# Kernel optimization log

Measured on AMD Instinct MI355X. Metric: run time of the kernel, lower is better.

The kernel has to match this reference:

```python
import jax, jax.numpy as jnp
import numpy as np

EPS = 1e-7  # K.epsilon()
ROUTINGS = 3
NUM_CAPSULE = 32
DIM_CAPSULE = 64


def squash(x, axis=-1):
    # NOTE: faithful to the source: x / sqrt(sum(x^2) + eps) (no squash factor)
    s = jnp.sum(jnp.square(x), axis=axis, keepdims=True)
    return x / jnp.sqrt(s + EPS)


def setup_inputs() -> dict:
    key = jax.random.key(0)
    k1, k2 = jax.random.split(key)
    B, I, C = 32, 1024, 256
    u_vecs = jax.random.normal(k1, (B, I, C), dtype=jnp.float32)
    # glorot-ish scale for the capsule kernel (1x1 conv == matmul C -> N*D)
    W = jax.random.normal(k2, (C, NUM_CAPSULE * DIM_CAPSULE), dtype=jnp.float32) * 0.03
    return {"u_vecs": u_vecs, "W": W}


def reference(u_vecs, W):
    B, I, C = u_vecs.shape
    N, D = NUM_CAPSULE, DIM_CAPSULE
    # conv1d with kernel size 1 == matmul; reshape + permute to (B, N, I, D)
    u_hat = jnp.einsum('bic,ce->bie', u_vecs, W)  # (B, I, N*D)
    u_hat = u_hat.reshape(B, I, N, D).transpose(0, 2, 1, 3)  # (B, N, I, D)

    b = jnp.zeros((B, N, I), dtype=u_hat.dtype)
    outputs = None
    for i in range(ROUTINGS):
        c = jax.nn.softmax(b, axis=1)  # softmax over num_capsule axis
        outputs = squash(jnp.einsum('bni,bnid->bnd', c, u_hat))  # (B, N, D)
        if i < ROUTINGS - 1:
            b = jnp.einsum('bnd,bnid->bni', outputs, u_hat)
    return outputs
```

## Files before the change

### kernel.cpp

```cpp
#include <hip/hip_runtime.h>
#include <math.h>


constexpr int Bn = 32, In = 1024, Cn = 256, Nn = 32, Dn = 64, ND = 2048;

typedef __attribute__((ext_vector_type(8))) short bf16x8;
typedef __attribute__((ext_vector_type(4))) float f32x4;

__device__ __forceinline__ unsigned int packbf2(float a, float b) {
  unsigned int xa = __float_as_uint(a), xb = __float_as_uint(b);
  xa = (xa + 0x7fffu + ((xa >> 16) & 1u)) >> 16;
  xb = (xb + 0x7fffu + ((xb >> 16) & 1u)) >> 16;
  return xa | (xb << 16);
}
__device__ __forceinline__ unsigned short packbf1(float a) {
  unsigned int x = __float_as_uint(a);
  return (unsigned short)((x + 0x7fffu + ((x >> 16) & 1u)) >> 16);
}
__device__ __forceinline__ float bfu(unsigned short us) {
  return __uint_as_float((unsigned int)us << 16);
}

__global__ __launch_bounds__(256) void k_pre(
    const float* __restrict__ u, const float* __restrict__ W,
    float* __restrict__ psu, unsigned short* __restrict__ Wbf,
    unsigned short* __restrict__ WbfT, unsigned short* __restrict__ ub16) {
  const int z = blockIdx.x, tid = threadIdx.x;
  if (z < 1024) {
    int b = z >> 5, ch = z & 31;
    const float* up = u + ((size_t)(b * In + ch * 32)) * Cn + tid;
    unsigned short* ubp = ub16 + ((size_t)(b * In + ch * 32)) * Cn + tid;
    float s = 0.f;
#pragma unroll 8
    for (int j = 0; j < 32; ++j) {
      float v = up[(size_t)j * Cn];
      s += v;
      ubp[(size_t)j * Cn] = packbf1(v);
    }
    psu[(size_t)z * Cn + tid] = s;
  } else if (z < 1152) {
    __shared__ float tile[64][65];
    int t = z - 1024;
    int x0 = (t & 31) * 64, y0 = (t >> 5) * 64;
    int lx = tid & 63, ly = tid >> 6;
#pragma unroll
    for (int k = 0; k < 16; ++k) {
      int y = ly + k * 4;
      tile[y][lx] = W[(size_t)(y0 + y) * ND + x0 + lx];
    }
    __syncthreads();
#pragma unroll
    for (int k = 0; k < 8; ++k) {
      int idx = tid + k * 256;
      int row = idx >> 5, cu = idx & 31;
      unsigned int v = packbf2(tile[2 * cu][row], tile[2 * cu + 1][row]);
      *(unsigned int*)&WbfT[(size_t)(x0 + row) * Cn + y0 + 2 * cu] = v;
    }
  } else {
    int zb = z - 1152;
    const float* src = W + (size_t)zb * 4096;
    unsigned short* dst = Wbf + (size_t)zb * 4096;
#pragma unroll
    for (int k = 0; k < 4; ++k) {
      int off = k * 1024 + tid * 4;
      const float4 v = *(const float4*)&src[off];
      *(uint2*)&dst[off] = make_uint2(packbf2(v.x, v.y), packbf2(v.z, v.w));
    }
  }
}

__global__ __launch_bounds__(256) void k_sst(
    const void* __restrict__ src, int srcBf16, long bS, long nS, long cS,
    float scale, const unsigned short* __restrict__ Wbf,
    const unsigned short* __restrict__ WbfT, unsigned short* __restrict__ tb,
    float* __restrict__ outp, int writeT) {
  int bn = blockIdx.x, b = bn >> 5, n = bn & 31;
  int tid = threadIdx.x;
  __shared__ float vs[Cn];
  __shared__ float ol[Dn];
  __shared__ float scr[2176];
  {
    const int g = tid >> 5, co = tid & 31;
    float acc[8];
#pragma unroll
    for (int e = 0; e < 8; ++e) acc[e] = 0.f;
    if (srcBf16) {
      const unsigned short* p =
          (const unsigned short*)src + b * bS + n * nS + co * 8;
#pragma unroll
      for (int k = 0; k < 4; ++k) {
        union { bf16x8 v; unsigned short us[8]; } w;
        w.v = *(const bf16x8*)&p[(size_t)(g * 4 + k) * cS];
#pragma unroll
        for (int e = 0; e < 8; ++e) acc[e] += bfu(w.us[e]);
      }
    } else {
      const float* p = (const float*)src + b * bS + n * nS + co * 8;
#pragma unroll
      for (int k = 0; k < 4; ++k) {
        const float4 v0 = *(const float4*)&p[(size_t)(g * 4 + k) * cS];
        const float4 v1 = *(const float4*)&p[(size_t)(g * 4 + k) * cS + 4];
        acc[0] += v0.x; acc[1] += v0.y; acc[2] += v0.z; acc[3] += v0.w;
        acc[4] += v1.x; acc[5] += v1.y; acc[6] += v1.z; acc[7] += v1.w;
      }
    }
    *(float4*)&scr[g * 272 + co * 8] =
        make_float4(acc[0], acc[1], acc[2], acc[3]);
    *(float4*)&scr[g * 272 + co * 8 + 4] =
        make_float4(acc[4], acc[5], acc[6], acc[7]);
  }
  __syncthreads();
  {
    float s = 0.f;
#pragma unroll
    for (int k = 0; k < 8; ++k) s += scr[k * 272 + tid];
    vs[tid] = s * scale;
  }
  __syncthreads();
  {
    const int cg = tid >> 3, do8 = tid & 7;
    const unsigned short* wp =
        Wbf + (size_t)(cg * 8) * ND + (size_t)n * Dn + do8 * 8;
    float acc[8];
#pragma unroll
    for (int e = 0; e < 8; ++e) acc[e] = 0.f;
#pragma unroll
    for (int j = 0; j < 8; ++j) {
      union { bf16x8 v; unsigned short us[8]; } w;
      w.v = *(const bf16x8*)&wp[(size_t)j * ND];
      const float vc = vs[cg * 8 + j];
#pragma unroll
      for (int e = 0; e < 8; ++e) acc[e] += vc * bfu(w.us[e]);
    }
    *(float4*)&scr[cg * 68 + do8 * 8] =
        make_float4(acc[0], acc[1], acc[2], acc[3]);
    *(float4*)&scr[cg * 68 + do8 * 8 + 4] =
        make_float4(acc[4], acc[5], acc[6], acc[7]);
  }
  __syncthreads();
  if (tid < 64) {
    float a = 0.f;
#pragma unroll
    for (int k = 0; k < 32; ++k) a += scr[k * 68 + tid];
    float sq = a * a;
#pragma unroll
    for (int off = 32; off > 0; off >>= 1) sq += __shfl_xor(sq, off, 64);
    float o = a / sqrtf(sq + 1e-7f);
    ol[tid] = o;
    if (outp) outp[(size_t)bn * Dn + tid] = o;
  }
  __syncthreads();
  if (writeT) {
    {
      const int dg = tid >> 5, co = tid & 31;
      const unsigned short* wt =
          WbfT + (size_t)(n * Dn + dg * 8) * Cn + co * 8;
      float acc[8];
#pragma unroll
      for (int e = 0; e < 8; ++e) acc[e] = 0.f;
#pragma unroll
      for (int e = 0; e < 8; ++e) {
        union { bf16x8 v; unsigned short us[8]; } w;
        w.v = *(const bf16x8*)&wt[(size_t)e * Cn];
        const float od = ol[dg * 8 + e];
#pragma unroll
        for (int cc = 0; cc < 8; ++cc) acc[cc] += od * bfu(w.us[cc]);
      }
      *(float4*)&scr[dg * 272 + co * 8] =
          make_float4(acc[0], acc[1], acc[2], acc[3]);
      *(float4*)&scr[dg * 272 + co * 8 + 4] =
          make_float4(acc[4], acc[5], acc[6], acc[7]);
    }
    __syncthreads();
    {
      float s = 0.f;
#pragma unroll
      for (int k = 0; k < 8; ++k) s += scr[k * 272 + tid];
      tb[(size_t)bn * Cn + tid] = packbf1(s);
    }
  }
}

__global__ __launch_bounds__(256, 4) void k_route(
    const unsigned short* __restrict__ tbb,
    const unsigned short* __restrict__ ub16,
    unsigned short* __restrict__ pvb) {
  const int b = blockIdx.x, itile = blockIdx.y, i0 = itile * 32;
  const int tid = threadIdx.x;
  const int lane = tid & 63, w = tid >> 6;
  const int mrow = lane & 15, quad = lane >> 4;

  __shared__ unsigned short t_l[32][264];
  __shared__ unsigned short u_t[256][40];
  __shared__ unsigned short cm_l[32][40];
  __shared__ float bb_l[32][36];
  __shared__ float smr[2][8][32];

  {
    const unsigned short* tp = tbb + (size_t)b * Nn * Cn;
#pragma unroll
    for (int k = 0; k < 8; ++k) {
      int idx = tid + k * 256;
      int row = idx >> 6, q = idx & 63;
      *(uint2*)&t_l[row][q * 4] = *(const uint2*)&tp[(size_t)row * Cn + q * 4];
    }
    const int ti = tid & 31, qb = tid >> 5;
    const unsigned short* up = ub16 + ((size_t)(b * In + i0 + ti)) * Cn;
#pragma unroll
    for (int m = 0; m < 4; ++m) {
      int c8 = qb + m * 8;
      union { bf16x8 v; unsigned short us[8]; } uv;
      uv.v = *(const bf16x8*)&up[c8 * 8];
#pragma unroll
      for (int e = 0; e < 8; ++e) u_t[c8 * 8 + e][ti] = uv.us[e];
    }
  }
  __syncthreads();

  {
    const int i0t = (w & 1) * 16, n0t = (w >> 1) * 16;
    const unsigned short* ubp =
        ub16 + ((size_t)(b * In + i0 + i0t + mrow)) * Cn + quad * 8;
    f32x4 acc = {0.f, 0.f, 0.f, 0.f};
#pragma unroll
    for (int k0 = 0; k0 < 8; ++k0) {
      const bf16x8 af = *(const bf16x8*)(ubp + k0 * 32);
      const bf16x8 bf = *(const bf16x8*)&t_l[n0t + mrow][k0 * 32 + quad * 8];
      acc = __builtin_amdgcn_mfma_f32_16x16x32_bf16(af, bf, acc, 0, 0, 0);
    }
#pragma unroll
    for (int r = 0; r < 4; ++r)
      bb_l[n0t + mrow][i0t + quad * 4 + r] = acc[r];
  }
  __syncthreads();

  {
    const int i = tid & 31, g = tid >> 5;
    float m4 = bb_l[g * 4 + 0][i];
    m4 = fmaxf(m4, bb_l[g * 4 + 1][i]);
    m4 = fmaxf(m4, bb_l[g * 4 + 2][i]);
    m4 = fmaxf(m4, bb_l[g * 4 + 3][i]);
    smr[0][g][i] = m4;
    __syncthreads();
    float m = smr[0][0][i];
#pragma unroll
    for (int k = 1; k < 8; ++k) m = fmaxf(m, smr[0][k][i]);
    float s4 = 0.f;
#pragma unroll
    for (int r = 0; r < 4; ++r) {
      float e = __expf(bb_l[g * 4 + r][i] - m);
      bb_l[g * 4 + r][i] = e;
      s4 += e;
    }
    smr[1][g][i] = s4;
    __syncthreads();
    float ss = 0.f;
#pragma unroll
    for (int k = 0; k < 8; ++k) ss += smr[1][k][i];
    float inv = 1.f / ss;
#pragma unroll
    for (int r = 0; r < 4; ++r) bb_l[g * 4 + r][i] *= inv;
  }
  __syncthreads();

  {
    int n = tid >> 3, q = tid & 7;
    const float4 cv = *(const float4*)&bb_l[n][q * 4];
    *(uint2*)&cm_l[n][q * 4] = make_uint2(packbf2(cv.x, cv.y), packbf2(cv.z, cv.w));
  }
  __syncthreads();

  unsigned short* pvs = &t_l[0][0];
  {
    const int mt = w & 1;
    const bf16x8 af = *(const bf16x8*)&cm_l[mt * 16 + mrow][quad * 8];
#pragma unroll
    for (int j = 0; j < 8; ++j) {
      const int ct = (w >> 1) * 8 + j;
      const bf16x8 bfv = *(const bf16x8*)&u_t[ct * 16 + mrow][quad * 8];
      f32x4 d = {0.f, 0.f, 0.f, 0.f};
      d = __builtin_amdgcn_mfma_f32_16x16x32_bf16(af, bfv, d, 0, 0, 0);
#pragma unroll
      for (int r = 0; r < 4; ++r)
        pvs[(size_t)(mt * 16 + quad * 4 + r) * 264 + ct * 16 + mrow] =
            packbf1(d[r]);
    }
  }
  __syncthreads();
  {
    unsigned short* pb = pvb + (size_t)((b * 32 + itile) * Nn) * Cn;
    const int rg = tid >> 5, co = tid & 31;
#pragma unroll
    for (int k = 0; k < 4; ++k) {
      int row = rg + k * 8;
      const uint4 v = *(const uint4*)&pvs[(size_t)row * 264 + co * 8];
      *(uint4*)&pb[(size_t)row * Cn + co * 8] = v;
    }
  }
}

extern "C" void kernel_launch(void* const* d_in, const int* in_sizes, int n_in,
                              void* d_out, int out_size, void* d_ws, size_t ws_size,
                              hipStream_t stream) {
  (void)in_sizes; (void)n_in; (void)out_size; (void)ws_size;
  const float* u = (const float*)d_in[0];
  const float* W = (const float*)d_in[1];
  float* out = (float*)d_out;
  float* ws = (float*)d_ws;
  unsigned short* pvb  = (unsigned short*)ws;
  float*          psu  = ws + 4194304;
  unsigned short* Wbf  = (unsigned short*)(ws + 4456448);
  unsigned short* WbfT = (unsigned short*)(ws + 4718592);
  unsigned short* tb16 = (unsigned short*)(ws + 4980736);
  unsigned short* ub16 = (unsigned short*)(ws + 5242880);

  k_pre<<<1280, 256, 0, stream>>>(u, W, psu, Wbf, WbfT, ub16);
  k_sst<<<1024, 256, 0, stream>>>(psu, 0, 8192L, 0L, 256L, 1.0f / 32.0f,
                                  Wbf, WbfT, tb16, nullptr, 1);
  k_route<<<dim3(32, 32), 256, 0, stream>>>(tb16, ub16, pvb);
  k_sst<<<1024, 256, 0, stream>>>(pvb, 1, 262144L, 256L, 8192L, 1.0f,
                                  Wbf, WbfT, tb16, nullptr, 1);
  k_route<<<dim3(32, 32), 256, 0, stream>>>(tb16, ub16, pvb);
  k_sst<<<1024, 256, 0, stream>>>(pvb, 1, 262144L, 256L, 8192L, 1.0f,
                                  Wbf, WbfT, tb16, out, 0);
}
```

Baseline: 126.8 us.

## Fuse squash and transform stage into routing kernel via last-block atomic counters

```diff
diff --git a/kernel.cpp b/kernel.cpp
--- a/kernel.cpp
+++ b/kernel.cpp
@@ -24,7 +24,8 @@
 __global__ __launch_bounds__(256) void k_pre(
     const float* __restrict__ u, const float* __restrict__ W,
     float* __restrict__ psu, unsigned short* __restrict__ Wbf,
-    unsigned short* __restrict__ WbfT, unsigned short* __restrict__ ub16) {
+    unsigned short* __restrict__ WbfT, unsigned short* __restrict__ ub16,
+    unsigned int* __restrict__ cnt) {
   const int z = blockIdx.x, tid = threadIdx.x;
   if (z < 1024) {
     int b = z >> 5, ch = z & 31;
@@ -58,6 +59,7 @@
     }
   } else {
     int zb = z - 1152;
+    if (zb == 0) { cnt[tid] = 0u; cnt[256 + tid] = 0u; }
     const float* src = W + (size_t)zb * 4096;
     unsigned short* dst = Wbf + (size_t)zb * 4096;
 #pragma unroll
@@ -70,10 +72,9 @@
 }
 
 __global__ __launch_bounds__(256) void k_sst(
-    const void* __restrict__ src, int srcBf16, long bS, long nS, long cS,
-    float scale, const unsigned short* __restrict__ Wbf,
-    const unsigned short* __restrict__ WbfT, unsigned short* __restrict__ tb,
-    float* __restrict__ outp, int writeT) {
+    const float* __restrict__ psu, float scale,
+    const unsigned short* __restrict__ Wbf,
+    const unsigned short* __restrict__ WbfT, unsigned short* __restrict__ tb) {
   int bn = blockIdx.x, b = bn >> 5, n = bn & 31;
   int tid = threadIdx.x;
   __shared__ float vs[Cn];
@@ -84,25 +85,13 @@
     float acc[8];
 #pragma unroll
     for (int e = 0; e < 8; ++e) acc[e] = 0.f;
-    if (srcBf16) {
-      const unsigned short* p =
-          (const unsigned short*)src + b * bS + n * nS + co * 8;
-#pragma unroll
-      for (int k = 0; k < 4; ++k) {
-        union { bf16x8 v; unsigned short us[8]; } w;
-        w.v = *(const bf16x8*)&p[(size_t)(g * 4 + k) * cS];
-#pragma unroll
-        for (int e = 0; e < 8; ++e) acc[e] += bfu(w.us[e]);
-      }
-    } else {
-      const float* p = (const float*)src + b * bS + n * nS + co * 8;
-#pragma unroll
-      for (int k = 0; k < 4; ++k) {
-        const float4 v0 = *(const float4*)&p[(size_t)(g * 4 + k) * cS];
-        const float4 v1 = *(const float4*)&p[(size_t)(g * 4 + k) * cS + 4];
-        acc[0] += v0.x; acc[1] += v0.y; acc[2] += v0.z; acc[3] += v0.w;
-        acc[4] += v1.x; acc[5] += v1.y; acc[6] += v1.z; acc[7] += v1.w;
-      }
+    const float* p = psu + (size_t)b * 8192 + co * 8;
+#pragma unroll
+    for (int k = 0; k < 4; ++k) {
+      const float4 v0 = *(const float4*)&p[(size_t)(g * 4 + k) * 256];
+      const float4 v1 = *(const float4*)&p[(size_t)(g * 4 + k) * 256 + 4];
+      acc[0] += v0.x; acc[1] += v0.y; acc[2] += v0.z; acc[3] += v0.w;
+      acc[4] += v1.x; acc[5] += v1.y; acc[6] += v1.z; acc[7] += v1.w;
     }
     *(float4*)&scr[g * 272 + co * 8] =
         make_float4(acc[0], acc[1], acc[2], acc[3]);
@@ -145,46 +134,45 @@
     float sq = a * a;
 #pragma unroll
     for (int off = 32; off > 0; off >>= 1) sq += __shfl_xor(sq, off, 64);
-    float o = a / sqrtf(sq + 1e-7f);
-    ol[tid] = o;
-    if (outp) outp[(size_t)bn * Dn + tid] = o;
-  }
-  __syncthreads();
-  if (writeT) {
-    {
-      const int dg = tid >> 5, co = tid & 31;
-      const unsigned short* wt =
-          WbfT + (size_t)(n * Dn + dg * 8) * Cn + co * 8;
-      float acc[8];
-#pragma unroll
-      for (int e = 0; e < 8; ++e) acc[e] = 0.f;
-#pragma unroll
-      for (int e = 0; e < 8; ++e) {
-        union { bf16x8 v; unsigned short us[8]; } w;
-        w.v = *(const bf16x8*)&wt[(size_t)e * Cn];
-        const float od = ol[dg * 8 + e];
-#pragma unroll
-        for (int cc = 0; cc < 8; ++cc) acc[cc] += od * bfu(w.us[cc]);
-      }
-      *(float4*)&scr[dg * 272 + co * 8] =
-          make_float4(acc[0], acc[1], acc[2], acc[3]);
-      *(float4*)&scr[dg * 272 + co * 8 + 4] =
-          make_float4(acc[4], acc[5], acc[6], acc[7]);
-    }
-    __syncthreads();
-    {
-      float s = 0.f;
-#pragma unroll
-      for (int k = 0; k < 8; ++k) s += scr[k * 272 + tid];
-      tb[(size_t)bn * Cn + tid] = packbf1(s);
-    }
-  }
-}
-
-__global__ __launch_bounds__(256, 4) void k_route(
+    ol[tid] = a / sqrtf(sq + 1e-7f);
+  }
+  __syncthreads();
+  {
+    const int dg = tid >> 5, co = tid & 31;
+    const unsigned short* wt = WbfT + (size_t)(n * Dn + dg * 8) * Cn + co * 8;
+    float acc[8];
+#pragma unroll
+    for (int e = 0; e < 8; ++e) acc[e] = 0.f;
+#pragma unroll
+    for (int e = 0; e < 8; ++e) {
+      union { bf16x8 v; unsigned short us[8]; } w;
+      w.v = *(const bf16x8*)&wt[(size_t)e * Cn];
+      const float od = ol[dg * 8 + e];
+#pragma unroll
+      for (int cc = 0; cc < 8; ++cc) acc[cc] += od * bfu(w.us[cc]);
+    }
+    *(float4*)&scr[dg * 272 + co * 8] =
+        make_float4(acc[0], acc[1], acc[2], acc[3]);
+    *(float4*)&scr[dg * 272 + co * 8 + 4] =
+        make_float4(acc[4], acc[5], acc[6], acc[7]);
+  }
+  __syncthreads();
+  {
+    float s = 0.f;
+#pragma unroll
+    for (int k = 0; k < 8; ++k) s += scr[k * 272 + tid];
+    tb[(size_t)bn * Cn + tid] = packbf1(s);
+  }
+}
+
+__global__ __launch_bounds__(256, 4) void k_route_f(
     const unsigned short* __restrict__ tbb,
     const unsigned short* __restrict__ ub16,
-    unsigned short* __restrict__ pvb) {
+    unsigned short* __restrict__ pvb,
+    const unsigned short* __restrict__ Wbf,
+    const unsigned short* __restrict__ WbfT,
+    unsigned short* __restrict__ t16_out, float* __restrict__ outp,
+    int writeT, unsigned int* __restrict__ cnt) {
   const int b = blockIdx.x, itile = blockIdx.y, i0 = itile * 32;
   const int tid = threadIdx.x;
   const int lane = tid & 63, w = tid >> 6;
@@ -195,6 +183,9 @@
   __shared__ unsigned short cm_l[32][40];
   __shared__ float bb_l[32][36];
   __shared__ float smr[2][8][32];
+  __shared__ unsigned int gmask;
+  __shared__ float vvL[4][256];
+  __shared__ float olL[4][64];
 
   {
     const unsigned short* tp = tbb + (size_t)b * Nn * Cn;
@@ -296,6 +287,95 @@
       const uint4 v = *(const uint4*)&pvs[(size_t)row * 264 + co * 8];
       *(uint4*)&pb[(size_t)row * Cn + co * 8] = v;
     }
+  }
+
+  __syncthreads();
+  if (tid == 0) {
+    __threadfence();
+    unsigned int m = 0;
+#pragma unroll
+    for (int g = 0; g < 8; ++g)
+      if (atomicAdd(&cnt[b * 8 + g], 1u) == 31u) m |= (1u << g);
+    gmask = m;
+  }
+  __syncthreads();
+  const unsigned int mask = gmask;
+  if (mask == 0) return;
+  __threadfence();
+
+  for (int g = 0; g < 8; ++g) {
+    if (!(mask & (1u << g))) continue;
+    const int n = g * 4 + w;
+    {
+      const unsigned short* p =
+          pvb + ((size_t)(b * 32) * 32 + n) * 256 + lane * 4;
+      float a0 = 0.f, a1 = 0.f, a2 = 0.f, a3 = 0.f;
+#pragma unroll
+      for (int it = 0; it < 32; ++it) {
+        uint2 r = *(const uint2*)&p[(size_t)it * 8192];
+        a0 += bfu((unsigned short)(r.x & 0xffffu));
+        a1 += bfu((unsigned short)(r.x >> 16));
+        a2 += bfu((unsigned short)(r.y & 0xffffu));
+        a3 += bfu((unsigned short)(r.y >> 16));
+      }
+      vvL[w][lane * 4 + 0] = a0; vvL[w][lane * 4 + 1] = a1;
+      vvL[w][lane * 4 + 2] = a2; vvL[w][lane * 4 + 3] = a3;
+    }
+    __syncthreads();
+    {
+      const int dg = lane & 7, cg = lane >> 3;
+      float acc[8];
+#pragma unroll
+      for (int e = 0; e < 8; ++e) acc[e] = 0.f;
+      const unsigned short* wp =
+          Wbf + (size_t)(cg * 32) * ND + (size_t)n * Dn + dg * 8;
+#pragma unroll
+      for (int j = 0; j < 32; ++j) {
+        union { bf16x8 v; unsigned short us[8]; } wv8;
+        wv8.v = *(const bf16x8*)&wp[(size_t)j * ND];
+        const float vc = vvL[w][cg * 32 + j];
+#pragma unroll
+        for (int e = 0; e < 8; ++e) acc[e] += vc * bfu(wv8.us[e]);
+      }
+#pragma unroll
+      for (int off = 8; off <= 32; off <<= 1)
+#pragma unroll
+        for (int e = 0; e < 8; ++e) acc[e] += __shfl_xor(acc[e], off, 64);
+      float sq = 0.f;
+#pragma unroll
+      for (int e = 0; e < 8; ++e) sq += acc[e] * acc[e];
+#pragma unroll
+      for (int off = 1; off <= 4; off <<= 1) sq += __shfl_xor(sq, off, 64);
+      const float inv = 1.0f / sqrtf(sq + 1e-7f);
+      if (cg == 0) {
+#pragma unroll
+        for (int e = 0; e < 8; ++e) {
+          float o = acc[e] * inv;
+          olL[w][dg * 8 + e] = o;
+          if (outp) outp[((size_t)(b * 32 + n)) * 64 + dg * 8 + e] = o;
+        }
+      }
+    }
+    __syncthreads();
+    if (writeT) {
+      float a[4];
+#pragma unroll
+      for (int e = 0; e < 4; ++e) a[e] = 0.f;
+      const unsigned short* wt = WbfT + ((size_t)(n * 64)) * Cn + lane * 4;
+#pragma unroll
+      for (int d = 0; d < 64; ++d) {
+        uint2 r = *(const uint2*)&wt[(size_t)d * Cn];
+        const float od = olL[w][d];
+        a[0] += od * bfu((unsigned short)(r.x & 0xffffu));
+        a[1] += od * bfu((unsigned short)(r.x >> 16));
+        a[2] += od * bfu((unsigned short)(r.y & 0xffffu));
+        a[3] += od * bfu((unsigned short)(r.y >> 16));
+      }
+      *(uint2*)&t16_out[((size_t)(b * 32 + n)) * Cn + lane * 4] = make_uint2(
+          ((unsigned int)packbf1(a[0])) | ((unsigned int)packbf1(a[1]) << 16),
+          ((unsigned int)packbf1(a[2])) | ((unsigned int)packbf1(a[3]) << 16));
+    }
+    __syncthreads();
   }
 }
 
@@ -313,14 +393,12 @@
   unsigned short* WbfT = (unsigned short*)(ws + 4718592);
   unsigned short* tb16 = (unsigned short*)(ws + 4980736);
   unsigned short* ub16 = (unsigned short*)(ws + 5242880);
-
-  k_pre<<<1280, 256, 0, stream>>>(u, W, psu, Wbf, WbfT, ub16);
-  k_sst<<<1024, 256, 0, stream>>>(psu, 0, 8192L, 0L, 256L, 1.0f / 32.0f,
-                                  Wbf, WbfT, tb16, nullptr, 1);
-  k_route<<<dim3(32, 32), 256, 0, stream>>>(tb16, ub16, pvb);
-  k_sst<<<1024, 256, 0, stream>>>(pvb, 1, 262144L, 256L, 8192L, 1.0f,
-                                  Wbf, WbfT, tb16, nullptr, 1);
-  k_route<<<dim3(32, 32), 256, 0, stream>>>(tb16, ub16, pvb);
-  k_sst<<<1024, 256, 0, stream>>>(pvb, 1, 262144L, 256L, 8192L, 1.0f,
-                                  Wbf, WbfT, tb16, out, 0);
-}
+  unsigned int*   cnt  = (unsigned int*)(ws + 9437184);
+
+  k_pre<<<1280, 256, 0, stream>>>(u, W, psu, Wbf, WbfT, ub16, cnt);
+  k_sst<<<1024, 256, 0, stream>>>(psu, 1.0f / 32.0f, Wbf, WbfT, tb16);
+  k_route_f<<<dim3(32, 32), 256, 0, stream>>>(tb16, ub16, pvb, Wbf, WbfT,
+                                              tb16, nullptr, 1, cnt);
+  k_route_f<<<dim3(32, 32), 256, 0, stream>>>(tb16, ub16, pvb, Wbf, WbfT,
+                                              nullptr, out, 0, cnt + 256);
+}
```

Result: slower. 280.3 us (+121.1%).
